# Performance work log

Measured on AMD Instinct MI355X. Metric: run time of the kernel, lower is better.

Reference implementation:

```python
import jax, jax.numpy as jnp
import numpy as np

N = 8192          # total nodes in the batch of graphs
ATOM = 64         # atom_feats
HID = 128         # hidden_feats
HEADS = 8         # num_heads
NUM_GRAPHS = 256  # number of graphs (max value of `batch`)
NEG_SLOPE = 0.2   # LeakyReLU slope in GAT attention


def setup_inputs() -> dict:
    key = jax.random.key(0)
    ks = jax.random.split(key, 16)
    x = jax.random.normal(ks[0], (N, ATOM), dtype=jnp.float32)
    adj = (jax.random.uniform(ks[1], (N, N)) < 0.01).astype(jnp.float32)
    adj = jnp.maximum(adj, jnp.eye(N, dtype=jnp.float32))
    batch = jnp.sort(jax.random.randint(ks[2], (N,), 0, NUM_GRAPHS)).astype(jnp.int32)

    def u(k, shape, fan_in):
        lim = 1.0 / np.sqrt(fan_in)
        return jax.random.uniform(k, shape, jnp.float32, -lim, lim)

    in1 = HID * HEADS
    params = dict(
        W0=u(ks[3], (ATOM, HID), ATOM), a0_src=u(ks[4], (HID,), HID), a0_dst=u(ks[5], (HID,), HID),
        W1=u(ks[6], (in1, HID), in1), a1_src=u(ks[7], (HID,), HID), a1_dst=u(ks[8], (HID,), HID),
        W2=u(ks[9], (in1, HID), in1), a2_src=u(ks[10], (HID,), HID), a2_dst=u(ks[11], (HID,), HID),
        fc_w=u(ks[12], (HID, 1), HID), fc_b=u(ks[13], (1,), HID),
    )
    return dict(x=x, adj=adj, batch=batch, **params)


def _gat_layer(h_in, W, a_src, a_dst, mask):
    # standard dense GAT: Wh, e_ij = leakyrelu(a_src.Wh_i + a_dst.Wh_j), masked softmax, aggregate
    h = h_in @ W                                         # [N, HID]
    e = jax.nn.leaky_relu((h @ a_src)[:, None] + (h @ a_dst)[None, :], NEG_SLOPE)  # [N, N]
    e = jnp.where(mask, e, jnp.float32(-1e9))
    attn = jax.nn.softmax(e, axis=1)                     # [N, N]
    return attn @ h                                      # [N, HID]


def reference(x, adj, batch, W0, a0_src, a0_dst, W1, a1_src, a1_dst, W2, a2_src, a2_dst, fc_w, fc_b):
    # eval mode: dropout is identity. The torch module calls the SAME layer instance per head,
    # so concat of heads == tile, and the final stacked mean == a single layer call.
    mask = adj > 0
    h0 = _gat_layer(x, W0, a0_src, a0_dst, mask)
    x1 = jax.nn.relu(jnp.tile(h0, (1, HEADS)))           # [N, HID*HEADS]
    h1 = _gat_layer(x1, W1, a1_src, a1_dst, mask)
    x2 = jax.nn.relu(jnp.tile(h1, (1, HEADS)))
    h2 = _gat_layer(x2, W2, a2_src, a2_dst, mask)        # mean over identical heads == h2
    # global mean pool over graphs
    sums = jax.ops.segment_sum(h2, batch, num_segments=NUM_GRAPHS)           # [G, HID]
    cnt = jax.ops.segment_sum(jnp.ones((N, 1), h2.dtype), batch, num_segments=NUM_GRAPHS)
    pooled = sums / jnp.maximum(cnt, 1.0)
    out = pooled @ fc_w + fc_b                           # [G, 1]
    return out[:, 0]
```

## Files before the change

### kernel.cpp

```cpp
#include <hip/hip_runtime.h>
#include <cstdint>
#include <cstddef>

#define NN 8192
#define ATOMF 64
#define HID 128
#define HEADS 8
#define NG 256
#define ELLW 192
#define NEGSLOPE 0.2f

__global__ __launch_bounds__(256) void k_build_ell(const float* __restrict__ adj,
                                                   int* __restrict__ ell,
                                                   int* __restrict__ deg) {
    int row = blockIdx.x;
    int t = threadIdx.x;
    const float4* a4 = (const float4*)(adj + (size_t)row * NN);
    float4 v[8];
    int c = 0;
    #pragma unroll
    for (int it = 0; it < 8; ++it) {
        v[it] = a4[it * 256 + t];
        c += (v[it].x > 0.f) + (v[it].y > 0.f) + (v[it].z > 0.f) + (v[it].w > 0.f);
    }
    __shared__ int cnt[256];
    cnt[t] = c;
    __syncthreads();
    for (int off = 1; off < 256; off <<= 1) {
        int x = (t >= off) ? cnt[t - off] : 0;
        __syncthreads();
        cnt[t] += x;
        __syncthreads();
    }
    int pos = cnt[t] - c;
    int total = cnt[255];
    int* er = ell + (size_t)row * ELLW;
    #pragma unroll
    for (int it = 0; it < 8; ++it) {
        int j0 = (it * 256 + t) * 4;
        if (v[it].x > 0.f && pos < ELLW) { er[pos] = j0;     ++pos; }
        if (v[it].y > 0.f && pos < ELLW) { er[pos] = j0 + 1; ++pos; }
        if (v[it].z > 0.f && pos < ELLW) { er[pos] = j0 + 2; ++pos; }
        if (v[it].w > 0.f && pos < ELLW) { er[pos] = j0 + 3; ++pos; }
    }
    if (t == 0) deg[row] = total < ELLW ? total : ELLW;
}

__global__ __launch_bounds__(256) void k_wreduce(const float* __restrict__ W,
                                                 float* __restrict__ Wr) {
    int i = blockIdx.x * 256 + threadIdx.x;
    if (i >= HID * HID) return;
    int k = i >> 7, c = i & 127;
    float s = 0.f;
    #pragma unroll
    for (int t = 0; t < HEADS; ++t)
        s += W[(size_t)(t * HID + k) * HID + c];
    Wr[i] = s;
}

template<int K, bool RELU>
__global__ __launch_bounds__(256) void k_gemm(const float* __restrict__ X,
                                              const float* __restrict__ W,
                                              float* __restrict__ Y) {
    __shared__ float Xl[32 * K];
    int t = threadIdx.x;
    int row0 = blockIdx.x * 32;
    for (int i = t; i < 32 * K; i += 256) {
        int r = i / K, k = i % K;
        float x = X[(size_t)(row0 + r) * K + k];
        Xl[i] = RELU ? fmaxf(x, 0.f) : x;
    }
    __syncthreads();
    int c = t & 127;
    int rh = t >> 7;
    float acc[16];
    #pragma unroll
    for (int m = 0; m < 16; ++m) acc[m] = 0.f;
    for (int k = 0; k < K; ++k) {
        float w = W[k * HID + c];
        #pragma unroll
        for (int m = 0; m < 16; ++m)
            acc[m] += Xl[(rh * 16 + m) * K + k] * w;
    }
    #pragma unroll
    for (int m = 0; m < 16; ++m)
        Y[(size_t)(row0 + rh * 16 + m) * HID + c] = acc[m];
}

__global__ __launch_bounds__(256) void k_scores(const float* __restrict__ h,
                                                const float* __restrict__ asrc,
                                                const float* __restrict__ adst,
                                                float* __restrict__ ssrc,
                                                float* __restrict__ sdst) {
    int wid = threadIdx.x >> 6;
    int lane = threadIdx.x & 63;
    int row = blockIdx.x * 4 + wid;
    const float* hr = h + (size_t)row * HID;
    float h0 = hr[lane], h1 = hr[lane + 64];
    float ps = h0 * asrc[lane] + h1 * asrc[lane + 64];
    float pd = h0 * adst[lane] + h1 * adst[lane + 64];
    #pragma unroll
    for (int o = 32; o; o >>= 1) {
        ps += __shfl_xor(ps, o);
        pd += __shfl_xor(pd, o);
    }
    if (lane == 0) { ssrc[row] = ps; sdst[row] = pd; }
}

__global__ __launch_bounds__(64) void k_agg(const float* __restrict__ h,
                                            const float* __restrict__ ssrc,
                                            const float* __restrict__ sdst,
                                            const int* __restrict__ ell,
                                            const int* __restrict__ deg,
                                            float* __restrict__ out) {
    __shared__ float wl[ELLW];
    __shared__ int jl[ELLW];
    int row = blockIdx.x;
    int l = threadIdx.x;
    int d = deg[row];
    float si = ssrc[row];
    const int* er = ell + (size_t)row * ELLW;
    float m = -1e30f;
    for (int k = l; k < d; k += 64) {
        int j = er[k];
        float e = si + sdst[j];
        e = e > 0.f ? e : NEGSLOPE * e;
        jl[k] = j; wl[k] = e;
        m = fmaxf(m, e);
    }
    #pragma unroll
    for (int o = 32; o; o >>= 1) m = fmaxf(m, __shfl_xor(m, o));
    float s = 0.f;
    for (int k = l; k < d; k += 64) {
        float w = __expf(wl[k] - m);
        wl[k] = w;
        s += w;
    }
    #pragma unroll
    for (int o = 32; o; o >>= 1) s += __shfl_xor(s, o);
    float inv = 1.f / s;
    __syncthreads();
    float a0 = 0.f, a1 = 0.f;
    for (int k = 0; k < d; ++k) {
        int j = jl[k];
        float w = wl[k];
        const float2 hv = *(const float2*)(h + (size_t)j * HID + 2 * l);
        a0 += w * hv.x; a1 += w * hv.y;
    }
    float2 o2; o2.x = a0 * inv; o2.y = a1 * inv;
    *(float2*)(out + (size_t)row * HID + 2 * l) = o2;
}

__global__ void k_zero(float* gsum, int* gcnt) {
    int t = blockIdx.x * 256 + threadIdx.x;
    if (t < NG) { gsum[t] = 0.f; gcnt[t] = 0; }
}

__global__ __launch_bounds__(256) void k_pool(const float* __restrict__ h,
                                              const int* __restrict__ batch,
                                              const float* __restrict__ fcw,
                                              float* __restrict__ gsum,
                                              int* __restrict__ gcnt) {
    int wid = threadIdx.x >> 6, lane = threadIdx.x & 63;
    int row = blockIdx.x * 4 + wid;
    const float* hr = h + (size_t)row * HID;
    float p = hr[lane] * fcw[lane] + hr[lane + 64] * fcw[lane + 64];
    #pragma unroll
    for (int o = 32; o; o >>= 1) p += __shfl_xor(p, o);
    if (lane == 0) {
        int g = batch[row];
        atomicAdd(&gsum[g], p);
        atomicAdd(&gcnt[g], 1);
    }
}

__global__ void k_final(const float* __restrict__ gsum, const int* __restrict__ gcnt,
                        const float* __restrict__ fcb, float* __restrict__ out) {
    int g = blockIdx.x * 256 + threadIdx.x;
    if (g < NG) out[g] = gsum[g] / fmaxf((float)gcnt[g], 1.f) + fcb[0];
}

extern "C" void kernel_launch(void* const* d_in, const int* in_sizes, int n_in,
                              void* d_out, int out_size, void* d_ws, size_t ws_size,
                              hipStream_t stream) {
    const float* x    = (const float*)d_in[0];
    const float* adj  = (const float*)d_in[1];
    const int*   batch= (const int*)  d_in[2];
    const float* W0   = (const float*)d_in[3];
    const float* a0s  = (const float*)d_in[4];
    const float* a0d  = (const float*)d_in[5];
    const float* W1   = (const float*)d_in[6];
    const float* a1s  = (const float*)d_in[7];
    const float* a1d  = (const float*)d_in[8];
    const float* W2   = (const float*)d_in[9];
    const float* a2s  = (const float*)d_in[10];
    const float* a2d  = (const float*)d_in[11];
    const float* fcw  = (const float*)d_in[12];
    const float* fcb  = (const float*)d_in[13];
    float* out = (float*)d_out;

    char* ws = (char*)d_ws;
    size_t off = 0;
    auto alloc = [&](size_t bytes) {
        char* p = ws + off;
        off = (off + bytes + 255) & ~255UL;
        return p;
    };
    int*   ell  = (int*)  alloc((size_t)NN * ELLW * 4);
    int*   deg  = (int*)  alloc((size_t)NN * 4);
    float* hA   = (float*)alloc((size_t)NN * HID * 4);
    float* hB   = (float*)alloc((size_t)NN * HID * 4);
    float* ssrc = (float*)alloc((size_t)NN * 4);
    float* sdst = (float*)alloc((size_t)NN * 4);
    float* Wr1  = (float*)alloc((size_t)HID * HID * 4);
    float* Wr2  = (float*)alloc((size_t)HID * HID * 4);
    float* gsum = (float*)alloc((size_t)NG * 4);
    int*   gcnt = (int*)  alloc((size_t)NG * 4);
    (void)ws_size; (void)in_sizes; (void)n_in; (void)out_size;

    k_build_ell<<<NN, 256, 0, stream>>>(adj, ell, deg);
    k_wreduce<<<64, 256, 0, stream>>>(W1, Wr1);
    k_wreduce<<<64, 256, 0, stream>>>(W2, Wr2);

    k_gemm<ATOMF, false><<<NN / 32, 256, 0, stream>>>(x, W0, hA);
    k_scores<<<NN / 4, 256, 0, stream>>>(hA, a0s, a0d, ssrc, sdst);
    k_agg<<<NN, 64, 0, stream>>>(hA, ssrc, sdst, ell, deg, hB);
    k_gemm<HID, true><<<NN / 32, 256, 0, stream>>>(hB, Wr1, hA);
    k_scores<<<NN / 4, 256, 0, stream>>>(hA, a1s, a1d, ssrc, sdst);
    k_agg<<<NN, 64, 0, stream>>>(hA, ssrc, sdst, ell, deg, hB);
    k_gemm<HID, true><<<NN / 32, 256, 0, stream>>>(hB, Wr2, hA);
    k_scores<<<NN / 4, 256, 0, stream>>>(hA, a2s, a2d, ssrc, sdst);
    k_agg<<<NN, 64, 0, stream>>>(hA, ssrc, sdst, ell, deg, hB);

    k_zero<<<1, 256, 0, stream>>>(gsum, gcnt);
    k_pool<<<NN / 4, 256, 0, stream>>>(hB, batch, fcw, gsum, gcnt);
    k_final<<<1, 256, 0, stream>>>(gsum, gcnt, fcb, out);
}
```

Before: 198.3 us.

## Fuse score computation into GEMM, batch aggregation rows, and fuse pooling

```diff
diff --git a/kernel.cpp b/kernel.cpp
--- a/kernel.cpp
+++ b/kernel.cpp
@@ -15,6 +15,7 @@
                                                    int* __restrict__ deg) {
     int row = blockIdx.x;
     int t = threadIdx.x;
+    int lane = t & 63, wid = t >> 6;
     const float4* a4 = (const float4*)(adj + (size_t)row * NN);
     float4 v[8];
     int c = 0;
@@ -23,47 +24,65 @@
         v[it] = a4[it * 256 + t];
         c += (v[it].x > 0.f) + (v[it].y > 0.f) + (v[it].z > 0.f) + (v[it].w > 0.f);
     }
-    __shared__ int cnt[256];
-    cnt[t] = c;
-    __syncthreads();
-    for (int off = 1; off < 256; off <<= 1) {
-        int x = (t >= off) ? cnt[t - off] : 0;
-        __syncthreads();
-        cnt[t] += x;
-        __syncthreads();
-    }
-    int pos = cnt[t] - c;
-    int total = cnt[255];
-    int* er = ell + (size_t)row * ELLW;
+    int s = c;
+    #pragma unroll
+    for (int o = 1; o < 64; o <<= 1) {
+        int u = __shfl_up(s, o);
+        if (lane >= o) s += u;
+    }
+    __shared__ int wtot[4];
+    if (lane == 63) wtot[wid] = s;
+    __syncthreads();
+    int offs = 0;
+    #pragma unroll
+    for (int w = 0; w < 4; ++w) offs += (w < wid) ? wtot[w] : 0;
+    int total = wtot[0] + wtot[1] + wtot[2] + wtot[3];
+    int pos = offs + s - c;
+
+    __shared__ int jls[ELLW];
     #pragma unroll
     for (int it = 0; it < 8; ++it) {
         int j0 = (it * 256 + t) * 4;
-        if (v[it].x > 0.f && pos < ELLW) { er[pos] = j0;     ++pos; }
-        if (v[it].y > 0.f && pos < ELLW) { er[pos] = j0 + 1; ++pos; }
-        if (v[it].z > 0.f && pos < ELLW) { er[pos] = j0 + 2; ++pos; }
-        if (v[it].w > 0.f && pos < ELLW) { er[pos] = j0 + 3; ++pos; }
-    }
-    if (t == 0) deg[row] = total < ELLW ? total : ELLW;
-}
-
-__global__ __launch_bounds__(256) void k_wreduce(const float* __restrict__ W,
-                                                 float* __restrict__ Wr) {
-    int i = blockIdx.x * 256 + threadIdx.x;
-    if (i >= HID * HID) return;
+        if (v[it].x > 0.f && pos < ELLW) { jls[pos] = j0;     ++pos; }
+        if (v[it].y > 0.f && pos < ELLW) { jls[pos] = j0 + 1; ++pos; }
+        if (v[it].z > 0.f && pos < ELLW) { jls[pos] = j0 + 2; ++pos; }
+        if (v[it].w > 0.f && pos < ELLW) { jls[pos] = j0 + 3; ++pos; }
+    }
+    __syncthreads();
+    int tot = total < ELLW ? total : ELLW;
+    int* er = ell + (size_t)row * ELLW;
+    for (int k = t; k < tot; k += 256) er[k] = jls[k];
+    if (t == 0) deg[row] = tot;
+}
+
+__global__ __launch_bounds__(256) void k_wreduce(const float* __restrict__ W1,
+                                                 const float* __restrict__ W2,
+                                                 float* __restrict__ Wr1,
+                                                 float* __restrict__ Wr2) {
+    int b = blockIdx.x;
+    const float* W = (b < 64) ? W1 : W2;
+    float* Wr = (b < 64) ? Wr1 : Wr2;
+    int i = (b & 63) * 256 + threadIdx.x;
     int k = i >> 7, c = i & 127;
     float s = 0.f;
     #pragma unroll
-    for (int t = 0; t < HEADS; ++t)
-        s += W[(size_t)(t * HID + k) * HID + c];
+    for (int h = 0; h < HEADS; ++h)
+        s += W[(size_t)(h * HID + k) * HID + c];
     Wr[i] = s;
 }
 
 template<int K, bool RELU>
-__global__ __launch_bounds__(256) void k_gemm(const float* __restrict__ X,
-                                              const float* __restrict__ W,
-                                              float* __restrict__ Y) {
+__global__ __launch_bounds__(256) void k_gemm_s(const float* __restrict__ X,
+                                                const float* __restrict__ W,
+                                                const float* __restrict__ asrc,
+                                                const float* __restrict__ adst,
+                                                float* __restrict__ Y,
+                                                float* __restrict__ ssrc,
+                                                float* __restrict__ sdst) {
     __shared__ float Xl[32 * K];
+    __shared__ float partS[4][16], partD[4][16];
     int t = threadIdx.x;
+    int lane = t & 63, w = t >> 6;
     int row0 = blockIdx.x * 32;
     for (int i = t; i < 32 * K; i += 256) {
         int r = i / K, k = i % K;
@@ -77,46 +96,42 @@
     #pragma unroll
     for (int m = 0; m < 16; ++m) acc[m] = 0.f;
     for (int k = 0; k < K; ++k) {
-        float w = W[k * HID + c];
+        float wv = W[k * HID + c];
         #pragma unroll
         for (int m = 0; m < 16; ++m)
-            acc[m] += Xl[(rh * 16 + m) * K + k] * w;
-    }
-    #pragma unroll
-    for (int m = 0; m < 16; ++m)
+            acc[m] += Xl[(rh * 16 + m) * K + k] * wv;
+    }
+    float as = asrc[c], ad = adst[c];
+    #pragma unroll
+    for (int m = 0; m < 16; ++m) {
         Y[(size_t)(row0 + rh * 16 + m) * HID + c] = acc[m];
-}
-
-__global__ __launch_bounds__(256) void k_scores(const float* __restrict__ h,
-                                                const float* __restrict__ asrc,
-                                                const float* __restrict__ adst,
-                                                float* __restrict__ ssrc,
-                                                float* __restrict__ sdst) {
+        float ps = acc[m] * as, pd = acc[m] * ad;
+        #pragma unroll
+        for (int o = 32; o; o >>= 1) {
+            ps += __shfl_xor(ps, o);
+            pd += __shfl_xor(pd, o);
+        }
+        if (lane == 0) { partS[w][m] = ps; partD[w][m] = pd; }
+    }
+    __syncthreads();
+    if (t < 32) {
+        int r2 = t >> 4, m = t & 15;
+        ssrc[row0 + t] = partS[2 * r2][m] + partS[2 * r2 + 1][m];
+        sdst[row0 + t] = partD[2 * r2][m] + partD[2 * r2 + 1][m];
+    }
+}
+
+__global__ __launch_bounds__(256) void k_agg(const float* __restrict__ h,
+                                             const float* __restrict__ ssrc,
+                                             const float* __restrict__ sdst,
+                                             const int* __restrict__ ell,
+                                             const int* __restrict__ deg,
+                                             float* __restrict__ out) {
+    __shared__ float wl[4][ELLW];
+    __shared__ int jl[4][ELLW];
     int wid = threadIdx.x >> 6;
-    int lane = threadIdx.x & 63;
+    int l = threadIdx.x & 63;
     int row = blockIdx.x * 4 + wid;
-    const float* hr = h + (size_t)row * HID;
-    float h0 = hr[lane], h1 = hr[lane + 64];
-    float ps = h0 * asrc[lane] + h1 * asrc[lane + 64];
-    float pd = h0 * adst[lane] + h1 * adst[lane + 64];
-    #pragma unroll
-    for (int o = 32; o; o >>= 1) {
-        ps += __shfl_xor(ps, o);
-        pd += __shfl_xor(pd, o);
-    }
-    if (lane == 0) { ssrc[row] = ps; sdst[row] = pd; }
-}
-
-__global__ __launch_bounds__(64) void k_agg(const float* __restrict__ h,
-                                            const float* __restrict__ ssrc,
-                                            const float* __restrict__ sdst,
-                                            const int* __restrict__ ell,
-                                            const int* __restrict__ deg,
-                                            float* __restrict__ out) {
-    __shared__ float wl[ELLW];
-    __shared__ int jl[ELLW];
-    int row = blockIdx.x;
-    int l = threadIdx.x;
     int d = deg[row];
     float si = ssrc[row];
     const int* er = ell + (size_t)row * ELLW;
@@ -125,59 +140,85 @@
         int j = er[k];
         float e = si + sdst[j];
         e = e > 0.f ? e : NEGSLOPE * e;
-        jl[k] = j; wl[k] = e;
+        jl[wid][k] = j; wl[wid][k] = e;
         m = fmaxf(m, e);
     }
     #pragma unroll
     for (int o = 32; o; o >>= 1) m = fmaxf(m, __shfl_xor(m, o));
     float s = 0.f;
     for (int k = l; k < d; k += 64) {
-        float w = __expf(wl[k] - m);
-        wl[k] = w;
+        float w = __expf(wl[wid][k] - m);
+        wl[wid][k] = w;
         s += w;
     }
     #pragma unroll
     for (int o = 32; o; o >>= 1) s += __shfl_xor(s, o);
     float inv = 1.f / s;
-    __syncthreads();
     float a0 = 0.f, a1 = 0.f;
-    for (int k = 0; k < d; ++k) {
-        int j = jl[k];
-        float w = wl[k];
-        const float2 hv = *(const float2*)(h + (size_t)j * HID + 2 * l);
-        a0 += w * hv.x; a1 += w * hv.y;
+    const float* h2l = h + 2 * l;
+    int k = 0;
+    for (; k + 4 <= d; k += 4) {
+        int j0 = jl[wid][k], j1 = jl[wid][k + 1], j2 = jl[wid][k + 2], j3 = jl[wid][k + 3];
+        float w0 = wl[wid][k], w1 = wl[wid][k + 1], w2 = wl[wid][k + 2], w3 = wl[wid][k + 3];
+        float2 v0 = *(const float2*)(h2l + (size_t)j0 * HID);
+        float2 v1 = *(const float2*)(h2l + (size_t)j1 * HID);
+        float2 v2 = *(const float2*)(h2l + (size_t)j2 * HID);
+        float2 v3 = *(const float2*)(h2l + (size_t)j3 * HID);
+        a0 += w0 * v0.x; a1 += w0 * v0.y;
+        a0 += w1 * v1.x; a1 += w1 * v1.y;
+        a0 += w2 * v2.x; a1 += w2 * v2.y;
+        a0 += w3 * v3.x; a1 += w3 * v3.y;
+    }
+    for (; k < d; ++k) {
+        int j = jl[wid][k];
+        float w = wl[wid][k];
+        float2 v = *(const float2*)(h2l + (size_t)j * HID);
+        a0 += w * v.x; a1 += w * v.y;
     }
     float2 o2; o2.x = a0 * inv; o2.y = a1 * inv;
     *(float2*)(out + (size_t)row * HID + 2 * l) = o2;
 }
 
-__global__ void k_zero(float* gsum, int* gcnt) {
-    int t = blockIdx.x * 256 + threadIdx.x;
-    if (t < NG) { gsum[t] = 0.f; gcnt[t] = 0; }
-}
-
-__global__ __launch_bounds__(256) void k_pool(const float* __restrict__ h,
-                                              const int* __restrict__ batch,
-                                              const float* __restrict__ fcw,
-                                              float* __restrict__ gsum,
-                                              int* __restrict__ gcnt) {
-    int wid = threadIdx.x >> 6, lane = threadIdx.x & 63;
-    int row = blockIdx.x * 4 + wid;
-    const float* hr = h + (size_t)row * HID;
-    float p = hr[lane] * fcw[lane] + hr[lane + 64] * fcw[lane + 64];
-    #pragma unroll
-    for (int o = 32; o; o >>= 1) p += __shfl_xor(p, o);
-    if (lane == 0) {
-        int g = batch[row];
-        atomicAdd(&gsum[g], p);
-        atomicAdd(&gcnt[g], 1);
-    }
-}
-
-__global__ void k_final(const float* __restrict__ gsum, const int* __restrict__ gcnt,
-                        const float* __restrict__ fcb, float* __restrict__ out) {
-    int g = blockIdx.x * 256 + threadIdx.x;
-    if (g < NG) out[g] = gsum[g] / fmaxf((float)gcnt[g], 1.f) + fcb[0];
+__global__ __launch_bounds__(256) void k_poolfc(const float* __restrict__ h,
+                                                const int* __restrict__ batch,
+                                                const float* __restrict__ fcw,
+                                                const float* __restrict__ fcb,
+                                                float* __restrict__ out) {
+    __shared__ float lsum[8];
+    __shared__ int lcnt[8];
+    int t = threadIdx.x;
+    int b = blockIdx.x;
+    int g0 = b * 8;
+    if (t < 8) { lsum[t] = 0.f; lcnt[t] = 0; }
+    int lo = 0, hi = NN;
+    for (int it = 0; it < 13; ++it) {
+        int mid = (lo + hi) >> 1;
+        if (batch[mid] < g0) lo = mid + 1; else hi = mid;
+    }
+    int lo2 = lo, hi2 = NN;
+    {
+        int a = lo, bb = NN;
+        for (int it = 0; it < 13; ++it) {
+            int mid = (a + bb) >> 1;
+            if (batch[mid] < g0 + 8) a = mid + 1; else bb = mid;
+        }
+        lo2 = lo; hi2 = a;
+    }
+    __syncthreads();
+    int wid = t >> 6, lane = t & 63;
+    for (int r = lo2 + wid; r < hi2; r += 4) {
+        const float* hr = h + (size_t)r * HID;
+        float p = hr[lane] * fcw[lane] + hr[lane + 64] * fcw[lane + 64];
+        #pragma unroll
+        for (int o = 32; o; o >>= 1) p += __shfl_xor(p, o);
+        if (lane == 0) {
+            int g = batch[r] - g0;
+            atomicAdd(&lsum[g], p);
+            atomicAdd(&lcnt[g], 1);
+        }
+    }
+    __syncthreads();
+    if (t < 8) out[g0 + t] = lsum[t] / fmaxf((float)lcnt[t], 1.f) + fcb[0];
 }
 
 extern "C" void kernel_launch(void* const* d_in, const int* in_sizes, int n_in,
@@ -214,25 +255,17 @@
     float* sdst = (float*)alloc((size_t)NN * 4);
     float* Wr1  = (float*)alloc((size_t)HID * HID * 4);
     float* Wr2  = (float*)alloc((size_t)HID * HID * 4);
-    float* gsum = (float*)alloc((size_t)NG * 4);
-    int*   gcnt = (int*)  alloc((size_t)NG * 4);
     (void)ws_size; (void)in_sizes; (void)n_in; (void)out_size;
 
     k_build_ell<<<NN, 256, 0, stream>>>(adj, ell, deg);
-    k_wreduce<<<64, 256, 0, stream>>>(W1, Wr1);
-    k_wreduce<<<64, 256, 0, stream>>>(W2, Wr2);
-
-    k_gemm<ATOMF, false><<<NN / 32, 256, 0, stream>>>(x, W0, hA);
-    k_scores<<<NN / 4, 256, 0, stream>>>(hA, a0s, a0d, ssrc, sdst);
-    k_agg<<<NN, 64, 0, stream>>>(hA, ssrc, sdst, ell, deg, hB);
-    k_gemm<HID, true><<<NN / 32, 256, 0, stream>>>(hB, Wr1, hA);
-    k_scores<<<NN / 4, 256, 0, stream>>>(hA, a1s, a1d, ssrc, sdst);
-    k_agg<<<NN, 64, 0, stream>>>(hA, ssrc, sdst, ell, deg, hB);
-    k_gemm<HID, true><<<NN / 32, 256, 0, stream>>>(hB, Wr2, hA);
-    k_scores<<<NN / 4, 256, 0, stream>>>(hA, a2s, a2d, ssrc, sdst);
-    k_agg<<<NN, 64, 0, stream>>>(hA, ssrc, sdst, ell, deg, hB);
-
-    k_zero<<<1, 256, 0, stream>>>(gsum, gcnt);
-    k_pool<<<NN / 4, 256, 0, stream>>>(hB, batch, fcw, gsum, gcnt);
-    k_final<<<1, 256, 0, stream>>>(gsum, gcnt, fcb, out);
-}
+    k_wreduce<<<128, 256, 0, stream>>>(W1, W2, Wr1, Wr2);
+
+    k_gemm_s<ATOMF, false><<<NN / 32, 256, 0, stream>>>(x, W0, a0s, a0d, hA, ssrc, sdst);
+    k_agg<<<NN / 4, 256, 0, stream>>>(hA, ssrc, sdst, ell, deg, hB);
+    k_gemm_s<HID, true><<<NN / 32, 256, 0, stream>>>(hB, Wr1, a1s, a1d, hA, ssrc, sdst);
+    k_agg<<<NN / 4, 256, 0, stream>>>(hA, ssrc, sdst, ell, deg, hB);
+    k_gemm_s<HID, true><<<NN / 32, 256, 0, stream>>>(hB, Wr2, a2s, a2d, hA, ssrc, sdst);
+    k_agg<<<NN / 4, 256, 0, stream>>>(hA, ssrc, sdst, ell, deg, hB);
+
+    k_poolfc<<<NG / 8, 256, 0, stream>>>(hB, batch, fcw, fcb, out);
+}
```

Result: slower. 225.4 us (+13.7%).

## Pack four rows per agg block, unroll gathers, fuse pooling and weight reduction

Applied to the files above, without the earlier changes.

```diff
diff --git a/kernel.cpp b/kernel.cpp
--- a/kernel.cpp
+++ b/kernel.cpp
@@ -46,15 +46,19 @@
     if (t == 0) deg[row] = total < ELLW ? total : ELLW;
 }
 
-__global__ __launch_bounds__(256) void k_wreduce(const float* __restrict__ W,
-                                                 float* __restrict__ Wr) {
-    int i = blockIdx.x * 256 + threadIdx.x;
-    if (i >= HID * HID) return;
+__global__ __launch_bounds__(256) void k_wreduce(const float* __restrict__ W1,
+                                                 const float* __restrict__ W2,
+                                                 float* __restrict__ Wr1,
+                                                 float* __restrict__ Wr2) {
+    int b = blockIdx.x;
+    const float* W = (b < 64) ? W1 : W2;
+    float* Wr = (b < 64) ? Wr1 : Wr2;
+    int i = (b & 63) * 256 + threadIdx.x;
     int k = i >> 7, c = i & 127;
     float s = 0.f;
     #pragma unroll
-    for (int t = 0; t < HEADS; ++t)
-        s += W[(size_t)(t * HID + k) * HID + c];
+    for (int h = 0; h < HEADS; ++h)
+        s += W[(size_t)(h * HID + k) * HID + c];
     Wr[i] = s;
 }
 
@@ -107,16 +111,19 @@
     if (lane == 0) { ssrc[row] = ps; sdst[row] = pd; }
 }
 
-__global__ __launch_bounds__(64) void k_agg(const float* __restrict__ h,
-                                            const float* __restrict__ ssrc,
-                                            const float* __restrict__ sdst,
-                                            const int* __restrict__ ell,
-                                            const int* __restrict__ deg,
-                                            float* __restrict__ out) {
-    __shared__ float wl[ELLW];
-    __shared__ int jl[ELLW];
-    int row = blockIdx.x;
-    int l = threadIdx.x;
+__global__ __launch_bounds__(256, 6) void k_agg(const float* __restrict__ h,
+                                                const float* __restrict__ ssrc,
+                                                const float* __restrict__ sdst,
+                                                const int* __restrict__ ell,
+                                                const int* __restrict__ deg,
+                                                float* __restrict__ out) {
+    __shared__ float wls[4][ELLW];
+    __shared__ int jls[4][ELLW];
+    int wid = threadIdx.x >> 6;
+    int l = threadIdx.x & 63;
+    int row = blockIdx.x * 4 + wid;
+    float* wl = wls[wid];
+    int* jl = jls[wid];
     int d = deg[row];
     float si = ssrc[row];
     const int* er = ell + (size_t)row * ELLW;
@@ -139,45 +146,62 @@
     #pragma unroll
     for (int o = 32; o; o >>= 1) s += __shfl_xor(s, o);
     float inv = 1.f / s;
-    __syncthreads();
     float a0 = 0.f, a1 = 0.f;
-    for (int k = 0; k < d; ++k) {
+    const float* h2l = h + 2 * l;
+    int k = 0;
+    for (; k + 8 <= d; k += 8) {
+        int j0 = jl[k],     j1 = jl[k + 1], j2 = jl[k + 2], j3 = jl[k + 3];
+        int j4 = jl[k + 4], j5 = jl[k + 5], j6 = jl[k + 6], j7 = jl[k + 7];
+        float w0 = wl[k],     w1 = wl[k + 1], w2 = wl[k + 2], w3 = wl[k + 3];
+        float w4 = wl[k + 4], w5 = wl[k + 5], w6 = wl[k + 6], w7 = wl[k + 7];
+        float2 v0 = *(const float2*)(h2l + (size_t)j0 * HID);
+        float2 v1 = *(const float2*)(h2l + (size_t)j1 * HID);
+        float2 v2 = *(const float2*)(h2l + (size_t)j2 * HID);
+        float2 v3 = *(const float2*)(h2l + (size_t)j3 * HID);
+        float2 v4 = *(const float2*)(h2l + (size_t)j4 * HID);
+        float2 v5 = *(const float2*)(h2l + (size_t)j5 * HID);
+        float2 v6 = *(const float2*)(h2l + (size_t)j6 * HID);
+        float2 v7 = *(const float2*)(h2l + (size_t)j7 * HID);
+        a0 += w0 * v0.x; a1 += w0 * v0.y;
+        a0 += w1 * v1.x; a1 += w1 * v1.y;
+        a0 += w2 * v2.x; a1 += w2 * v2.y;
+        a0 += w3 * v3.x; a1 += w3 * v3.y;
+        a0 += w4 * v4.x; a1 += w4 * v4.y;
+        a0 += w5 * v5.x; a1 += w5 * v5.y;
+        a0 += w6 * v6.x; a1 += w6 * v6.y;
+        a0 += w7 * v7.x; a1 += w7 * v7.y;
+    }
+    for (; k < d; ++k) {
         int j = jl[k];
         float w = wl[k];
-        const float2 hv = *(const float2*)(h + (size_t)j * HID + 2 * l);
-        a0 += w * hv.x; a1 += w * hv.y;
+        float2 v = *(const float2*)(h2l + (size_t)j * HID);
+        a0 += w * v.x; a1 += w * v.y;
     }
     float2 o2; o2.x = a0 * inv; o2.y = a1 * inv;
     *(float2*)(out + (size_t)row * HID + 2 * l) = o2;
 }
 
-__global__ void k_zero(float* gsum, int* gcnt) {
-    int t = blockIdx.x * 256 + threadIdx.x;
-    if (t < NG) { gsum[t] = 0.f; gcnt[t] = 0; }
-}
-
-__global__ __launch_bounds__(256) void k_pool(const float* __restrict__ h,
-                                              const int* __restrict__ batch,
-                                              const float* __restrict__ fcw,
-                                              float* __restrict__ gsum,
-                                              int* __restrict__ gcnt) {
-    int wid = threadIdx.x >> 6, lane = threadIdx.x & 63;
-    int row = blockIdx.x * 4 + wid;
-    const float* hr = h + (size_t)row * HID;
-    float p = hr[lane] * fcw[lane] + hr[lane + 64] * fcw[lane + 64];
-    #pragma unroll
-    for (int o = 32; o; o >>= 1) p += __shfl_xor(p, o);
-    if (lane == 0) {
-        int g = batch[row];
-        atomicAdd(&gsum[g], p);
-        atomicAdd(&gcnt[g], 1);
-    }
-}
-
-__global__ void k_final(const float* __restrict__ gsum, const int* __restrict__ gcnt,
-                        const float* __restrict__ fcb, float* __restrict__ out) {
-    int g = blockIdx.x * 256 + threadIdx.x;
-    if (g < NG) out[g] = gsum[g] / fmaxf((float)gcnt[g], 1.f) + fcb[0];
+__global__ __launch_bounds__(256) void k_poolfc(const float* __restrict__ h,
+                                                const int* __restrict__ batch,
+                                                const float* __restrict__ fcw,
+                                                const float* __restrict__ fcb,
+                                                float* __restrict__ out) {
+    int wid = threadIdx.x >> 6, l = threadIdx.x & 63;
+    int g = blockIdx.x * 4 + wid;
+    int lo = 0, hi = NN;
+    while (lo < hi) { int mid = (lo + hi) >> 1; if (batch[mid] < g) lo = mid + 1; else hi = mid; }
+    int e0 = lo;
+    hi = NN;
+    while (lo < hi) { int mid = (lo + hi) >> 1; if (batch[mid] <= g) lo = mid + 1; else hi = mid; }
+    int e1 = lo;
+    float sum = 0.f;
+    for (int r = e0; r < e1; ++r) {
+        const float* hr = h + (size_t)r * HID;
+        sum += hr[l] * fcw[l] + hr[l + 64] * fcw[l + 64];
+    }
+    #pragma unroll
+    for (int o = 32; o; o >>= 1) sum += __shfl_xor(sum, o);
+    if (l == 0) out[g] = sum / fmaxf((float)(e1 - e0), 1.f) + fcb[0];
 }
 
 extern "C" void kernel_launch(void* const* d_in, const int* in_sizes, int n_in,
@@ -214,25 +238,20 @@
     float* sdst = (float*)alloc((size_t)NN * 4);
     float* Wr1  = (float*)alloc((size_t)HID * HID * 4);
     float* Wr2  = (float*)alloc((size_t)HID * HID * 4);
-    float* gsum = (float*)alloc((size_t)NG * 4);
-    int*   gcnt = (int*)  alloc((size_t)NG * 4);
     (void)ws_size; (void)in_sizes; (void)n_in; (void)out_size;
 
     k_build_ell<<<NN, 256, 0, stream>>>(adj, ell, deg);
-    k_wreduce<<<64, 256, 0, stream>>>(W1, Wr1);
-    k_wreduce<<<64, 256, 0, stream>>>(W2, Wr2);
+    k_wreduce<<<128, 256, 0, stream>>>(W1, W2, Wr1, Wr2);
 
     k_gemm<ATOMF, false><<<NN / 32, 256, 0, stream>>>(x, W0, hA);
     k_scores<<<NN / 4, 256, 0, stream>>>(hA, a0s, a0d, ssrc, sdst);
-    k_agg<<<NN, 64, 0, stream>>>(hA, ssrc, sdst, ell, deg, hB);
+    k_agg<<<NN / 4, 256, 0, stream>>>(hA, ssrc, sdst, ell, deg, hB);
     k_gemm<HID, true><<<NN / 32, 256, 0, stream>>>(hB, Wr1, hA);
     k_scores<<<NN / 4, 256, 0, stream>>>(hA, a1s, a1d, ssrc, sdst);
-    k_agg<<<NN, 64, 0, stream>>>(hA, ssrc, sdst, ell, deg, hB);
+    k_agg<<<NN / 4, 256, 0, stream>>>(hA, ssrc, sdst, ell, deg, hB);
     k_gemm<HID, true><<<NN / 32, 256, 0, stream>>>(hB, Wr2, hA);
     k_scores<<<NN / 4, 256, 0, stream>>>(hA, a2s, a2d, ssrc, sdst);
-    k_agg<<<NN, 64, 0, stream>>>(hA, ssrc, sdst, ell, deg, hB);
-
-    k_zero<<<1, 256, 0, stream>>>(gsum, gcnt);
-    k_pool<<<NN / 4, 256, 0, stream>>>(hB, batch, fcw, gsum, gcnt);
-    k_final<<<1, 256, 0, stream>>>(gsum, gcnt, fcb, out);
-}
+    k_agg<<<NN / 4, 256, 0, stream>>>(hA, ssrc, sdst, ell, deg, hB);
+
+    k_poolfc<<<NG / 4, 256, 0, stream>>>(hB, batch, fcw, fcb, out);
+}
```

After: 201.9 us. About the same (+1.8%).
